# Performance work log

Measured on AMD Instinct MI355X. Metric: run time of the kernel, lower is better.

## Reference

```python
import jax, jax.numpy as jnp
import numpy as np

SIGMA = 2.0


def _level(h, centers, W, b):
    # h: [n_prev, d], centers: [n_cur, d], W: [d, d] (torch Linear weight), b: [d]
    # squared distances via expansion: ||h||^2 - 2 h.c + ||c||^2  -> [n_prev, n_cur]
    sq = (jnp.sum(h * h, axis=1, keepdims=True)
          - 2.0 * (h @ centers.T)
          + jnp.sum(centers * centers, axis=1)[None, :])
    p = jax.nn.softmax(-sq / (2.0 * SIGMA), axis=1)  # softmax over centers per row
    t = jnp.tanh(h @ W.T + b)                        # [n_prev, d]
    # h_next[i] = sum_j p[j, i] * t[j]
    return p.T @ t                                   # [n_cur, d]


def setup_inputs() -> dict:
    key = jax.random.key(0)
    ks = jax.random.split(key, 11)
    d = 1024
    num_centers = [16384, 2048, 256, 32]
    inp = {"task_embedding": jax.random.normal(ks[0], (num_centers[0], d), dtype=jnp.float32)}
    # cluster centers per level (torch.rand -> uniform [0,1))
    inp["centers1"] = jax.random.uniform(ks[1], (num_centers[1], d), dtype=jnp.float32)
    inp["centers2"] = jax.random.uniform(ks[2], (num_centers[2], d), dtype=jnp.float32)
    inp["centers3"] = jax.random.uniform(ks[3], (num_centers[3], d), dtype=jnp.float32)
    # linear layers (Kaiming-uniform-ish init bound)
    bound = 1.0 / np.sqrt(d)
    for i, kw, kb in [(1, ks[4], ks[5]), (2, ks[6], ks[7]), (3, ks[8], ks[9])]:
        inp[f"W{i}"] = jax.random.uniform(kw, (d, d), minval=-bound, maxval=bound, dtype=jnp.float32)
        inp[f"b{i}"] = jax.random.uniform(kb, (d,), minval=-bound, maxval=bound, dtype=jnp.float32)
    return inp


def reference(task_embedding, centers1, centers2, centers3, W1, b1, W2, b2, W3, b3):
    h = task_embedding
    h = _level(h, centers1, W1, b1)
    h = _level(h, centers2, W2, b2)
    h = _level(h, centers3, W3, b3)
    return h
```

## Files before the change

kernel.cpp:

```cpp
#include <hip/hip_runtime.h>
#include <cmath>

typedef _Float16 half8 __attribute__((ext_vector_type(8)));
typedef _Float16 half4v __attribute__((ext_vector_type(4)));
typedef __attribute__((ext_vector_type(4))) float floatx4;

#define GLOAD_LDS16(gp, lp)                                            \
  __builtin_amdgcn_global_load_lds(                                    \
      (const __attribute__((address_space(1))) void*)(gp),             \
      (__attribute__((address_space(3))) void*)(lp), 16, 0, 0)

static inline int cdiv(int a, int b) { return (a + b - 1) / b; }


__global__ void prep(const float* __restrict__ h0, const float* __restrict__ W1,
                     const float* __restrict__ W2, const float* __restrict__ W3,
                     const float* __restrict__ c1, const float* __restrict__ c2,
                     const float* __restrict__ c3,
                     _Float16* __restrict__ hh, _Float16* __restrict__ Wh1,
                     _Float16* __restrict__ Wh2, _Float16* __restrict__ Wh3,
                     _Float16* __restrict__ cb1, _Float16* __restrict__ cb2,
                     _Float16* __restrict__ cb3,
                     float* __restrict__ cn1, float* __restrict__ cn2,
                     float* __restrict__ cn3,
                     int nh, int nw, int castBlocks, int n1, int n2) {
  int t = threadIdx.x;
  if ((int)blockIdx.x < castBlocks) {
    int gi = (blockIdx.x * 256 + t) * 4;
    const float* src; _Float16* dst; int off;
    if (gi < nh)                { src = h0; dst = hh;  off = gi; }
    else if (gi < nh + nw)      { src = W1; dst = Wh1; off = gi - nh; }
    else if (gi < nh + 2 * nw)  { src = W2; dst = Wh2; off = gi - nh - nw; }
    else if (gi < nh + 3 * nw)  { src = W3; dst = Wh3; off = gi - nh - 2 * nw; }
    else return;
    float4 v = *(const float4*)(src + off);
    half4v o = {(_Float16)v.x, (_Float16)v.y, (_Float16)v.z, (_Float16)v.w};
    *(half4v*)(dst + off) = o;
    return;
  }
  int row = blockIdx.x - castBlocks;
  const float* c; _Float16* cb; float* cn;
  if (row < n1)            { c = c1; cb = cb1; cn = cn1; }
  else if (row < n1 + n2)  { row -= n1; c = c2; cb = cb2; cn = cn2; }
  else                     { row -= n1 + n2; c = c3; cb = cb3; cn = cn3; }
  float4 v = *(const float4*)(c + (size_t)row * 1024 + t * 4);
  half4v o = {(_Float16)v.x, (_Float16)v.y, (_Float16)v.z, (_Float16)v.w};
  *(half4v*)(cb + (size_t)row * 1024 + t * 4) = o;
  float s = v.x * v.x + v.y * v.y + v.z * v.z + v.w * v.w;
  #pragma unroll
  for (int off = 32; off > 0; off >>= 1) s += __shfl_down(s, off, 64);
  __shared__ float ws[4];
  if ((t & 63) == 0) ws[t >> 6] = s;
  __syncthreads();
  if (t == 0) cn[row] = ws[0] + ws[1] + ws[2] + ws[3];
}

#define SM_CHUNK 64
__global__ void colexp_partial(_Float16* __restrict__ ST, const float* __restrict__ pmax,
                               float* __restrict__ psum, int mchunks, int ncur, int nprev) {
  int col = (blockIdx.x * 256 + threadIdx.x) * 4;
  if (col >= nprev) return;
  float m0 = -1e30f, m1 = -1e30f, m2 = -1e30f, m3 = -1e30f;
  for (int k = 0; k < mchunks; ++k) {
    float4 v = *(const float4*)(pmax + (size_t)k * nprev + col);
    m0 = fmaxf(m0, v.x); m1 = fmaxf(m1, v.y); m2 = fmaxf(m2, v.z); m3 = fmaxf(m3, v.w);
  }
  int j0 = blockIdx.y * SM_CHUNK;
  int j1 = min(j0 + SM_CHUNK, ncur);
  float s0 = 0.f, s1 = 0.f, s2 = 0.f, s3 = 0.f;
  for (int j = j0; j < j1; ++j) {
    size_t o = (size_t)j * nprev + col;
    half4v x = *(const half4v*)(ST + o);
    float e0 = __expf((float)x[0] - m0), e1 = __expf((float)x[1] - m1);
    float e2 = __expf((float)x[2] - m2), e3 = __expf((float)x[3] - m3);
    half4v e = {(_Float16)e0, (_Float16)e1, (_Float16)e2, (_Float16)e3};
    *(half4v*)(ST + o) = e;
    s0 += e0; s1 += e1; s2 += e2; s3 += e3;
  }
  float4 sv = {s0, s1, s2, s3};
  *(float4*)(psum + (size_t)blockIdx.y * nprev + col) = sv;
}

__global__ void reduce_parts(const _Float16* __restrict__ part, _Float16* __restrict__ out,
                             int mn, int S) {
  int i = (blockIdx.x * 256 + threadIdx.x) * 4;
  if (i >= mn) return;
  float a0 = 0.f, a1 = 0.f, a2 = 0.f, a3 = 0.f;
  for (int s = 0; s < S; ++s) {
    half4v v = *(const half4v*)(part + (size_t)s * mn + i);
    a0 += (float)v[0]; a1 += (float)v[1]; a2 += (float)v[2]; a3 += (float)v[3];
  }
  half4v o = {(_Float16)a0, (_Float16)a1, (_Float16)a2, (_Float16)a3};
  *(half4v*)(out + i) = o;
}

enum { EP_LOGIT = 0, EP_TANH = 1, EP_TANHP = 2, EP_F16 = 3, EP_F32 = 4, EP_PART = 5 };

template<int BM, int BN, int EPI>
__device__ __forceinline__ void gemm_body(
    const _Float16* __restrict__ A, const _Float16* __restrict__ B,
    void* __restrict__ Cout,
    const float* __restrict__ aux1,
    const float* __restrict__ aux2,
    float* __restrict__ pmax,
    int pnchunks,
    int M, int N, int K, int kLen,
    int bx, int by, int bz,
    _Float16* As, _Float16* Bs) {
  constexpr int BK = 64;
  constexpr int WTM = BM / 2, WTN = BN / 2;
  constexpr int FM = WTM / 16, FN = WTN / 16;
  float* smf = (float*)As;
  const int tid  = threadIdx.x;
  const int lane = tid & 63;
  const int wave = tid >> 6;
  const int wm = wave >> 1, wn = wave & 1;
  const int mBase = bx * BM, nBase = by * BN;
  const int kBase = bz * kLen;
  const int lr    = lane & 15;
  const int kHalf = (lane >> 4) << 3;

  const int srOff  = lane >> 3;
  const int schunk = (lane & 7) ^ srOff;
  floatx4 acc[FM][FN] = {};
  constexpr int AV = BM * BK / (256 * 8);
  constexpr int BV = BN * BK / (256 * 8);

  for (int k0 = kBase; k0 < kBase + kLen; k0 += BK) {
    #pragma unroll
    for (int v = 0; v < AV; ++v) {
      int rowBase = v * 32 + wave * 8;
      int gm = mBase + rowBase + srOff;
      if (gm >= M) gm = M - 1;
      GLOAD_LDS16(A + (size_t)gm * K + k0 + schunk * 8, &As[rowBase * BK]);
    }
    #pragma unroll
    for (int v = 0; v < BV; ++v) {
      int rowBase = v * 32 + wave * 8;
      int gn = nBase + rowBase + srOff;
      if (gn >= N) gn = N - 1;
      GLOAD_LDS16(B + (size_t)gn * K + k0 + schunk * 8, &Bs[rowBase * BK]);
    }
    __syncthreads();
    #pragma unroll
    for (int kk = 0; kk < BK; kk += 32) {
      const int q = (kk + kHalf) >> 3;
      half8 af[FM], bfv[FN];
      #pragma unroll
      for (int i = 0; i < FM; ++i) {
        int r = wm * WTM + i * 16 + lr;
        af[i] = *(const half8*)(&As[r * BK + ((q ^ (r & 7)) << 3)]);
      }
      #pragma unroll
      for (int j = 0; j < FN; ++j) {
        int r = wn * WTN + j * 16 + lr;
        bfv[j] = *(const half8*)(&Bs[r * BK + ((q ^ (r & 7)) << 3)]);
      }
      #pragma unroll
      for (int i = 0; i < FM; ++i)
        #pragma unroll
        for (int j = 0; j < FN; ++j)
          acc[i][j] = __builtin_amdgcn_mfma_f32_16x16x32_f16(af[i], bfv[j], acc[i][j], 0, 0, 0);
    }
    __syncthreads();
  }

  if (EPI == EP_TANH) {
    if (tid < BN) {
      int col = nBase + tid;
      float ssum = 0.f;
      if (col < N)
        for (int k = 0; k < pnchunks; ++k) ssum += aux2[(size_t)k * N + col];
      smf[tid] = 1.f / ssum;
    }
    __syncthreads();
  }

  const int rBase = (lane >> 4) << 2;
  float lmax[FN];
  #pragma unroll
  for (int j = 0; j < FN; ++j) lmax[j] = -1e30f;
  #pragma unroll
  for (int i = 0; i < FM; ++i) {
    #pragma unroll
    for (int j = 0; j < FN; ++j) {
      #pragma unroll
      for (int r = 0; r < 4; ++r) {
        int row = mBase + wm * WTM + i * 16 + rBase + r;
        int col = nBase + wn * WTN + j * 16 + lr;
        if (row < M && col < N) {
          float v = acc[i][j][r];
          size_t o = (size_t)row * N + col;
          if (EPI == EP_LOGIT) {
            v = 0.5f * v - 0.25f * aux1[row];
            ((_Float16*)Cout)[o] = (_Float16)v;
            lmax[j] = fmaxf(lmax[j], v);
          } else if (EPI == EP_TANH) {
            v = tanhf(v + aux1[row]) * smf[col - nBase];
            ((_Float16*)Cout)[o] = (_Float16)v;
          } else if (EPI == EP_TANHP) {
            v = tanhf(v + aux1[row]);
            ((_Float16*)Cout)[o] = (_Float16)v;
          } else if (EPI == EP_F16) {
            ((_Float16*)Cout)[o] = (_Float16)v;
          } else if (EPI == EP_PART) {
            ((_Float16*)Cout)[(size_t)bz * M * N + o] = (_Float16)v;
          } else {
            ((float*)Cout)[o] = v;
          }
        }
      }
    }
  }
  if (EPI == EP_LOGIT) {
    #pragma unroll
    for (int j = 0; j < FN; ++j) {
      float m = lmax[j];
      m = fmaxf(m, __shfl_xor(m, 16, 64));
      m = fmaxf(m, __shfl_xor(m, 32, 64));
      if ((lane >> 4) == 0) smf[wm * BN + wn * WTN + j * 16 + lr] = m;
    }
    __syncthreads();
    if (tid < BN) {
      int col = nBase + tid;
      if (col < N)
        pmax[(size_t)bx * N + col] = fmaxf(smf[tid], smf[BN + tid]);
    }
  }
}

template<int BM, int BN, int EPI>
__launch_bounds__(256, 4)
__global__ void gemm_nt(const _Float16* __restrict__ A, const _Float16* __restrict__ B,
                        void* __restrict__ Cout, const float* __restrict__ aux1,
                        const float* __restrict__ aux2, float* __restrict__ pmax,
                        int pnchunks, int M, int N, int K, int kLen) {
  __shared__ __align__(16) _Float16 As[BM * 64];
  __shared__ __align__(16) _Float16 Bs[BN * 64];
  gemm_body<BM, BN, EPI>(A, B, Cout, aux1, aux2, pmax, pnchunks, M, N, K, kLen,
                         blockIdx.x, blockIdx.y, blockIdx.z, As, Bs);
}

template<int BM, int BN>
__device__ __forceinline__ void fused_ls_body(
    const _Float16* __restrict__ A,
    const _Float16* __restrict__ B,
    _Float16* __restrict__ Eout,
    const float* __restrict__ cn,
    int M, int N, int K, int nBase,
    char* smem, float* redm, float* reds) {
  constexpr int BK = 64;
  constexpr int WTM = BM / 2, WTN = BN / 2;
  constexpr int FM = WTM / 16, FN = WTN / 16;
  constexpr int TLD = BN + 4;
  _Float16* As = (_Float16*)smem;
  _Float16* Bs = As + BM * BK;
  float* tile = (float*)smem;
  const int tid  = threadIdx.x;
  const int lane = tid & 63;
  const int wave = tid >> 6;
  const int wm = wave >> 1, wn = wave & 1;
  const int lr    = lane & 15;
  const int kHalf = (lane >> 4) << 3;
  const int srOff  = lane >> 3;
  const int schunk = (lane & 7) ^ srOff;
  floatx4 acc[FM][FN] = {};
  constexpr int AV = BM * BK / (256 * 8);
  constexpr int BV = BN * BK / (256 * 8);

  for (int k0 = 0; k0 < K; k0 += BK) {
    #pragma unroll
    for (int v = 0; v < AV; ++v) {
      int rowBase = v * 32 + wave * 8;
      GLOAD_LDS16(A + (size_t)(rowBase + srOff) * K + k0 + schunk * 8, &As[rowBase * BK]);
    }
    #pragma unroll
    for (int v = 0; v < BV; ++v) {
      int rowBase = v * 32 + wave * 8;
      GLOAD_LDS16(B + (size_t)(nBase + rowBase + srOff) * K + k0 + schunk * 8, &Bs[rowBase * BK]);
    }
    __syncthreads();
    #pragma unroll
    for (int kk = 0; kk < BK; kk += 32) {
      const int q = (kk + kHalf) >> 3;
      half8 af[FM], bfv[FN];
      #pragma unroll
      for (int i = 0; i < FM; ++i) {
        int r = wm * WTM + i * 16 + lr;
        af[i] = *(const half8*)(&As[r * BK + ((q ^ (r & 7)) << 3)]);
      }
      #pragma unroll
      for (int j = 0; j < FN; ++j) {
        int r = wn * WTN + j * 16 + lr;
        bfv[j] = *(const half8*)(&Bs[r * BK + ((q ^ (r & 7)) << 3)]);
      }
      #pragma unroll
      for (int i = 0; i < FM; ++i)
        #pragma unroll
        for (int j = 0; j < FN; ++j)
          acc[i][j] = __builtin_amdgcn_mfma_f32_16x16x32_f16(af[i], bfv[j], acc[i][j], 0, 0, 0);
    }
    __syncthreads();
  }

  const int rBase = (lane >> 4) << 2;
  #pragma unroll
  for (int i = 0; i < FM; ++i)
    #pragma unroll
    for (int j = 0; j < FN; ++j)
      #pragma unroll
      for (int r = 0; r < 4; ++r) {
        int row = wm * WTM + i * 16 + rBase + r;
        int col = wn * WTN + j * 16 + lr;
        tile[row * TLD + col] = 0.5f * acc[i][j][r] - 0.25f * cn[row];
      }
  __syncthreads();

  constexpr int P = 256 / BN;
  const int c = tid & (BN - 1);
  const int p = tid / BN;
  float m = -1e30f;
  for (int j = p; j < M; j += P) m = fmaxf(m, tile[j * TLD + c]);
  redm[p * BN + c] = m;
  __syncthreads();
  float mf = redm[c];
  #pragma unroll
  for (int q = 1; q < P; ++q) mf = fmaxf(mf, redm[q * BN + c]);
  float s = 0.f;
  for (int j = p; j < M; j += P) {
    float e = __expf(tile[j * TLD + c] - mf);
    tile[j * TLD + c] = e;
    s += e;
  }
  reds[p * BN + c] = s;
  __syncthreads();
  float l = 0.f;
  #pragma unroll
  for (int q = 0; q < P; ++q) l += reds[q * BN + c];
  const float li = 1.f / l;
  for (int j = p; j < M; j += P)
    Eout[(size_t)j * N + nBase + c] = (_Float16)(tile[j * TLD + c] * li);
}

__launch_bounds__(256, 2)
__global__ void lvl2_merged(const _Float16* __restrict__ cb2,
                            const _Float16* __restrict__ h1b,
                            _Float16* __restrict__ E, const float* __restrict__ cn2,
                            const _Float16* __restrict__ Wb2,
                            _Float16* __restrict__ tT, const float* __restrict__ b2) {
  __shared__ __align__(16) char smem[38912];
  if ((int)blockIdx.x < 64) {
    float* redm = (float*)(smem + 36864);
    float* reds = (float*)(smem + 36864 + 1024);
    fused_ls_body<256, 32>(cb2, h1b, E, cn2, 256, 2048, 1024, blockIdx.x * 32,
                           smem, redm, reds);
  } else {
    int lin = blockIdx.x - 64;
    gemm_body<128, 64, EP_TANHP>(Wb2, h1b, tT, b2, nullptr, nullptr, 0,
                                 1024, 2048, 1024, 1024, lin % 8, lin / 8, 0,
                                 (_Float16*)smem, (_Float16*)(smem + 16384));
  }
}

__launch_bounds__(256, 2)
__global__ void lvl3_merged(const _Float16* __restrict__ cb3,
                            const _Float16* __restrict__ h2b,
                            _Float16* __restrict__ E, const float* __restrict__ cn3,
                            const _Float16* __restrict__ Wb3,
                            _Float16* __restrict__ tT, const float* __restrict__ b3) {
  __shared__ __align__(16) char smem[16384];
  if ((int)blockIdx.x < 4) {
    float* redm = (float*)(smem + 12288);
    float* reds = (float*)(smem + 12288 + 1024);
    fused_ls_body<32, 64>(cb3, h2b, E, cn3, 32, 256, 1024, blockIdx.x * 64,
                          smem, redm, reds);
  } else {
    int lin = blockIdx.x - 4;
    gemm_body<64, 64, EP_TANHP>(Wb3, h2b, tT, b3, nullptr, nullptr, 0,
                                1024, 256, 1024, 1024, lin % 16, lin / 16, 0,
                                (_Float16*)smem, (_Float16*)(smem + 8192));
  }
}

extern "C" void kernel_launch(void* const* d_in, const int* in_sizes, int n_in,
                              void* d_out, int out_size, void* d_ws, size_t ws_size,
                              hipStream_t stream) {
  const float* h0 = (const float*)d_in[0];
  const float* c1 = (const float*)d_in[1];
  const float* c2 = (const float*)d_in[2];
  const float* c3 = (const float*)d_in[3];
  const float* W1 = (const float*)d_in[4];
  const float* b1 = (const float*)d_in[5];
  const float* W2 = (const float*)d_in[6];
  const float* b2 = (const float*)d_in[7];
  const float* W3 = (const float*)d_in[8];
  const float* b3 = (const float*)d_in[9];

  const int d = 1024;
  const int N0 = 16384, N1 = 2048, N2 = 256, N3 = 32;

  char* w = (char*)d_ws;
  size_t off = 0;
  auto alloc = [&](size_t bytes) {
    void* p = w + off;
    off += (bytes + 255) & ~(size_t)255;
    return p;
  };
  _Float16* hb  = (_Float16*)alloc((size_t)N0 * d * 2);
  _Float16* cb1 = (_Float16*)alloc((size_t)N1 * d * 2);
  _Float16* cb2 = (_Float16*)alloc((size_t)N2 * d * 2);
  _Float16* cb3 = (_Float16*)alloc((size_t)N3 * d * 2);
  float* cn1 = (float*)alloc((size_t)N1 * 4);
  float* cn2 = (float*)alloc((size_t)N2 * 4);
  float* cn3 = (float*)alloc((size_t)N3 * 4);
  _Float16* Wb1 = (_Float16*)alloc((size_t)d * d * 2);
  _Float16* Wb2 = (_Float16*)alloc((size_t)d * d * 2);
  _Float16* Wb3 = (_Float16*)alloc((size_t)d * d * 2);
  _Float16* ST = (_Float16*)alloc((size_t)N1 * N0 * 2);
  _Float16* tT = (_Float16*)alloc((size_t)d * N0 * 2);
  float* pmax = (float*)alloc((size_t)32 * N0 * 4);
  float* psum = (float*)alloc((size_t)32 * N0 * 4);
  _Float16* h1b = (_Float16*)alloc((size_t)N1 * d * 2);
  _Float16* h2b = (_Float16*)alloc((size_t)N2 * d * 2);
  _Float16* Cpart = (_Float16*)alloc((size_t)8 * N1 * d * 2);
  _Float16* E = ST;
  (void)ws_size; (void)in_sizes; (void)n_in; (void)out_size;

  int nh = N0 * d, nw = d * d;
  int castBlocks = cdiv(nh + 3 * nw, 1024);
  prep<<<castBlocks + N1 + N2 + N3, 256, 0, stream>>>(
      h0, W1, W2, W3, c1, c2, c3, hb, Wb1, Wb2, Wb3, cb1, cb2, cb3,
      cn1, cn2, cn3, nh, nw, castBlocks, N1, N2);

  gemm_nt<128, 128, EP_LOGIT><<<dim3(16, 128), 256, 0, stream>>>(
      cb1, hb, ST, cn1, nullptr, pmax, 0, N1, N0, d, d);
  colexp_partial<<<dim3(N0 / 1024, cdiv(N1, SM_CHUNK)), 256, 0, stream>>>(
      ST, pmax, psum, 16, N1, N0);
  gemm_nt<128, 128, EP_TANH><<<dim3(8, 128), 256, 0, stream>>>(
      Wb1, hb, tT, b1, psum, nullptr, cdiv(N1, SM_CHUNK), d, N0, d, d);
  gemm_nt<128, 128, EP_PART><<<dim3(16, 8, 8), 256, 0, stream>>>(
      E, tT, Cpart, nullptr, nullptr, nullptr, 0, N1, d, N0, N0 / 8);
  reduce_parts<<<cdiv(N1 * d, 1024), 256, 0, stream>>>(Cpart, h1b, N1 * d, 8);

  lvl2_merged<<<64 + 256, 256, 0, stream>>>(cb2, h1b, E, cn2, Wb2, tT, b2);
  gemm_nt<64, 64, EP_PART><<<dim3(4, 16, 8), 256, 0, stream>>>(
      E, tT, Cpart, nullptr, nullptr, nullptr, 0, N2, d, N1, N1 / 8);
  reduce_parts<<<cdiv(N2 * d, 1024), 256, 0, stream>>>(Cpart, h2b, N2 * d, 8);

  lvl3_merged<<<4 + 64, 256, 0, stream>>>(cb3, h2b, E, cn3, Wb3, tT, b3);
  gemm_nt<64, 64, EP_F32><<<dim3(1, 16), 256, 0, stream>>>(
      E, tT, d_out, nullptr, nullptr, nullptr, 0, N3, d, N2, N2);
}
```

Baseline: 454.8 us.

## Fuse level-1 logit and tanh GEMMs into one launch over stacked weights

```diff
diff --git a/kernel.cpp b/kernel.cpp
--- a/kernel.cpp
+++ b/kernel.cpp
@@ -81,6 +81,27 @@
   *(float4*)(psum + (size_t)blockIdx.y * nprev + col) = sv;
 }
 
+__global__ void tscale(_Float16* __restrict__ tT, const float* __restrict__ psum,
+                       int pnchunks, int N0) {
+  __shared__ float linv[256];
+  const int t = threadIdx.x;
+  const int c0 = blockIdx.x * 256;
+  float s = 0.f;
+  for (int k = 0; k < pnchunks; ++k) s += psum[(size_t)k * N0 + c0 + t];
+  linv[t] = 1.f / s;
+  __syncthreads();
+  const int cc = (t & 63) * 4;
+  const float4 li = *(const float4*)&linv[cc];
+  const int r0 = blockIdx.y * 64 + (t >> 6) * 16;
+  for (int r = r0; r < r0 + 16; ++r) {
+    size_t o = (size_t)r * N0 + c0 + cc;
+    half4v v = *(const half4v*)(tT + o);
+    half4v ov = {(_Float16)((float)v[0] * li.x), (_Float16)((float)v[1] * li.y),
+                 (_Float16)((float)v[2] * li.z), (_Float16)((float)v[3] * li.w)};
+    *(half4v*)(tT + o) = ov;
+  }
+}
+
 __global__ void reduce_parts(const _Float16* __restrict__ part, _Float16* __restrict__ out,
                              int mn, int S) {
   int i = (blockIdx.x * 256 + threadIdx.x) * 4;
@@ -94,7 +115,8 @@
   *(half4v*)(out + i) = o;
 }
 
-enum { EP_LOGIT = 0, EP_TANH = 1, EP_TANHP = 2, EP_F16 = 3, EP_F32 = 4, EP_PART = 5 };
+enum { EP_LOGIT = 0, EP_TANH = 1, EP_TANHP = 2, EP_F16 = 3, EP_F32 = 4, EP_PART = 5,
+       EP_LT = 6 };
 
 template<int BM, int BN, int EPI>
 __device__ __forceinline__ void gemm_body(
@@ -106,6 +128,7 @@
     int pnchunks,
     int M, int N, int K, int kLen,
     int bx, int by, int bz,
+    void* __restrict__ Cout2,
     _Float16* As, _Float16* Bs) {
   constexpr int BK = 64;
   constexpr int WTM = BM / 2, WTN = BN / 2;
@@ -177,6 +200,50 @@
   }
 
   const int rBase = (lane >> 4) << 2;
+  if (EPI == EP_LT) {
+    const int Ms = pnchunks;
+    if (mBase < Ms) {
+      float lmax[FN];
+      #pragma unroll
+      for (int j = 0; j < FN; ++j) lmax[j] = -1e30f;
+      #pragma unroll
+      for (int i = 0; i < FM; ++i)
+        #pragma unroll
+        for (int j = 0; j < FN; ++j)
+          #pragma unroll
+          for (int r = 0; r < 4; ++r) {
+            int row = mBase + wm * WTM + i * 16 + rBase + r;
+            int col = nBase + wn * WTN + j * 16 + lr;
+            float v = 0.5f * acc[i][j][r] - 0.25f * aux1[row];
+            ((_Float16*)Cout)[(size_t)row * N + col] = (_Float16)v;
+            lmax[j] = fmaxf(lmax[j], v);
+          }
+      #pragma unroll
+      for (int j = 0; j < FN; ++j) {
+        float m = lmax[j];
+        m = fmaxf(m, __shfl_xor(m, 16, 64));
+        m = fmaxf(m, __shfl_xor(m, 32, 64));
+        if ((lane >> 4) == 0) smf[wm * BN + wn * WTN + j * 16 + lr] = m;
+      }
+      __syncthreads();
+      if (tid < BN)
+        pmax[(size_t)bx * N + nBase + tid] = fmaxf(smf[tid], smf[BN + tid]);
+    } else {
+      _Float16* t2 = (_Float16*)Cout2;
+      #pragma unroll
+      for (int i = 0; i < FM; ++i)
+        #pragma unroll
+        for (int j = 0; j < FN; ++j)
+          #pragma unroll
+          for (int r = 0; r < 4; ++r) {
+            int row = mBase - Ms + wm * WTM + i * 16 + rBase + r;
+            int col = nBase + wn * WTN + j * 16 + lr;
+            float v = tanhf(acc[i][j][r] + aux2[row]);
+            t2[(size_t)row * N + col] = (_Float16)v;
+          }
+    }
+    return;
+  }
   float lmax[FN];
   #pragma unroll
   for (int j = 0; j < FN; ++j) lmax[j] = -1e30f;
@@ -234,11 +301,12 @@
 __global__ void gemm_nt(const _Float16* __restrict__ A, const _Float16* __restrict__ B,
                         void* __restrict__ Cout, const float* __restrict__ aux1,
                         const float* __restrict__ aux2, float* __restrict__ pmax,
-                        int pnchunks, int M, int N, int K, int kLen) {
+                        int pnchunks, int M, int N, int K, int kLen,
+                        void* __restrict__ Cout2) {
   __shared__ __align__(16) _Float16 As[BM * 64];
   __shared__ __align__(16) _Float16 Bs[BN * 64];
   gemm_body<BM, BN, EPI>(A, B, Cout, aux1, aux2, pmax, pnchunks, M, N, K, kLen,
-                         blockIdx.x, blockIdx.y, blockIdx.z, As, Bs);
+                         blockIdx.x, blockIdx.y, blockIdx.z, Cout2, As, Bs);
 }
 
 template<int BM, int BN>
@@ -358,7 +426,7 @@
     int lin = blockIdx.x - 64;
     gemm_body<128, 64, EP_TANHP>(Wb2, h1b, tT, b2, nullptr, nullptr, 0,
                                  1024, 2048, 1024, 1024, lin % 8, lin / 8, 0,
-                                 (_Float16*)smem, (_Float16*)(smem + 16384));
+                                 nullptr, (_Float16*)smem, (_Float16*)(smem + 16384));
   }
 }
 
@@ -378,7 +446,7 @@
     int lin = blockIdx.x - 4;
     gemm_body<64, 64, EP_TANHP>(Wb3, h2b, tT, b3, nullptr, nullptr, 0,
                                 1024, 256, 1024, 1024, lin % 16, lin / 16, 0,
-                                (_Float16*)smem, (_Float16*)(smem + 8192));
+                                nullptr, (_Float16*)smem, (_Float16*)(smem + 8192));
   }
 }
 
@@ -407,13 +475,14 @@
     return p;
   };
   _Float16* hb  = (_Float16*)alloc((size_t)N0 * d * 2);
-  _Float16* cb1 = (_Float16*)alloc((size_t)N1 * d * 2);
+  _Float16* A1  = (_Float16*)alloc((size_t)(N1 + d) * d * 2);
+  _Float16* cb1 = A1;
+  _Float16* Wb1 = A1 + (size_t)N1 * d;
   _Float16* cb2 = (_Float16*)alloc((size_t)N2 * d * 2);
   _Float16* cb3 = (_Float16*)alloc((size_t)N3 * d * 2);
   float* cn1 = (float*)alloc((size_t)N1 * 4);
   float* cn2 = (float*)alloc((size_t)N2 * 4);
   float* cn3 = (float*)alloc((size_t)N3 * 4);
-  _Float16* Wb1 = (_Float16*)alloc((size_t)d * d * 2);
   _Float16* Wb2 = (_Float16*)alloc((size_t)d * d * 2);
   _Float16* Wb3 = (_Float16*)alloc((size_t)d * d * 2);
   _Float16* ST = (_Float16*)alloc((size_t)N1 * N0 * 2);
@@ -432,22 +501,21 @@
       h0, W1, W2, W3, c1, c2, c3, hb, Wb1, Wb2, Wb3, cb1, cb2, cb3,
       cn1, cn2, cn3, nh, nw, castBlocks, N1, N2);
 
-  gemm_nt<128, 128, EP_LOGIT><<<dim3(16, 128), 256, 0, stream>>>(
-      cb1, hb, ST, cn1, nullptr, pmax, 0, N1, N0, d, d);
+  gemm_nt<128, 128, EP_LT><<<dim3((N1 + d) / 128, N0 / 128), 256, 0, stream>>>(
+      A1, hb, ST, cn1, b1, pmax, N1, N1 + d, N0, d, d, tT);
   colexp_partial<<<dim3(N0 / 1024, cdiv(N1, SM_CHUNK)), 256, 0, stream>>>(
-      ST, pmax, psum, 16, N1, N0);
-  gemm_nt<128, 128, EP_TANH><<<dim3(8, 128), 256, 0, stream>>>(
-      Wb1, hb, tT, b1, psum, nullptr, cdiv(N1, SM_CHUNK), d, N0, d, d);
+      ST, pmax, psum, N1 / 128, N1, N0);
+  tscale<<<dim3(N0 / 256, d / 64), 256, 0, stream>>>(tT, psum, cdiv(N1, SM_CHUNK), N0);
   gemm_nt<128, 128, EP_PART><<<dim3(16, 8, 8), 256, 0, stream>>>(
-      E, tT, Cpart, nullptr, nullptr, nullptr, 0, N1, d, N0, N0 / 8);
+      E, tT, Cpart, nullptr, nullptr, nullptr, 0, N1, d, N0, N0 / 8, nullptr);
   reduce_parts<<<cdiv(N1 * d, 1024), 256, 0, stream>>>(Cpart, h1b, N1 * d, 8);
 
   lvl2_merged<<<64 + 256, 256, 0, stream>>>(cb2, h1b, E, cn2, Wb2, tT, b2);
   gemm_nt<64, 64, EP_PART><<<dim3(4, 16, 8), 256, 0, stream>>>(
-      E, tT, Cpart, nullptr, nullptr, nullptr, 0, N2, d, N1, N1 / 8);
+      E, tT, Cpart, nullptr, nullptr, nullptr, 0, N2, d, N1, N1 / 8, nullptr);
   reduce_parts<<<cdiv(N2 * d, 1024), 256, 0, stream>>>(Cpart, h2b, N2 * d, 8);
 
   lvl3_merged<<<4 + 64, 256, 0, stream>>>(cb3, h2b, E, cn3, Wb3, tT, b3);
   gemm_nt<64, 64, EP_F32><<<dim3(1, 16), 256, 0, stream>>>(
-      E, tT, d_out, nullptr, nullptr, nullptr, 0, N3, d, N2, N2);
-}
+      E, tT, d_out, nullptr, nullptr, nullptr, 0, N3, d, N2, N2, nullptr);
+}
```

After: 426.8 us. 6.2% less time.
